# Kernel tuning notes

Hardware: AMD Instinct MI355X
Metric: run time of the kernel (lower is better)

## Reference

```python
import jax, jax.numpy as jnp
import numpy as np

B, T, C, H = 2, 2048, 1024, 16
HD = C // H  # head dim = 64


def setup_inputs() -> dict:
    key = jax.random.key(0)
    ks = jax.random.split(key, 5)
    s = 1.0 / np.sqrt(C)
    return {
        "x": jax.random.normal(ks[0], (B, T, C), dtype=jnp.float32),
        "Wq": jax.random.normal(ks[1], (C, C), dtype=jnp.float32) * s,
        "bq": jnp.zeros((C,), dtype=jnp.float32),
        "Wk": jax.random.normal(ks[2], (C, C), dtype=jnp.float32) * s,
        "bk": jnp.zeros((C,), dtype=jnp.float32),
        "Wv": jax.random.normal(ks[3], (C, C), dtype=jnp.float32) * s,
        "bv": jnp.zeros((C,), dtype=jnp.float32),
        "Wp": jax.random.normal(ks[4], (C, C), dtype=jnp.float32) * s,
        "bp": jnp.zeros((C,), dtype=jnp.float32),
    }


def reference(x, Wq, bq, Wk, bk, Wv, bv, Wp, bp):
    # QKV projections -> [B, H, T, HD]
    def proj(W, b):
        return (x @ W.T + b).reshape(B, T, H, HD).transpose(0, 2, 1, 3)

    q = proj(Wq, bq)
    k = proj(Wk, bk)
    v = proj(Wv, bv)

    scale = 1.0 / np.sqrt(HD)
    att = jnp.einsum("bhtd,bhsd->bhts", q, k) * scale  # [B,H,T,T]
    causal = jnp.tril(jnp.ones((T, T), dtype=bool))
    att = jnp.where(causal, att, -jnp.inf)
    att = jax.nn.softmax(att, axis=-1)
    y = jnp.einsum("bhts,bhsd->bhtd", att, v)          # [B,H,T,HD]
    y = y.transpose(0, 2, 1, 3).reshape(B, T, C)
    return y @ Wp.T + bp
```

## Files before the change

### kernel.cpp

```cpp
#include <hip/hip_runtime.h>
#include <hip/hip_bf16.h>

#define BB 2
#define TT 2048
#define CC 1024
#define HH 16
#define HDD 64

typedef __attribute__((ext_vector_type(8))) short bf16x8;
typedef __attribute__((ext_vector_type(4))) float f32x4;

static __device__ __forceinline__ unsigned short f2bf(float f) {
  union { float f; unsigned u; } v; v.f = f;
  unsigned r = v.u + 0x7fffu + ((v.u >> 16) & 1u);
  return (unsigned short)(r >> 16);
}

static __device__ __forceinline__ unsigned fbits(float f) {
  union { float f; unsigned u; } v; v.f = f; return v.u;
}

static __device__ __forceinline__ unsigned pk_trunc(float lo, float hi) {
  return __builtin_amdgcn_perm(fbits(hi), fbits(lo), 0x07060302u);
}

static __device__ __forceinline__ void gload_lds16(const unsigned short* g, unsigned short* l) {
  __builtin_amdgcn_global_load_lds((const __attribute__((address_space(1))) void*)g,
                                   (__attribute__((address_space(3))) void*)l, 16, 0, 0);
}

__global__ __launch_bounds__(256) void convert_all(
    const float* __restrict__ x, const float* __restrict__ Wq,
    const float* __restrict__ Wk, const float* __restrict__ Wv,
    const float* __restrict__ Wp, unsigned short* __restrict__ dst)
{
  const size_t M4 = 4194304, M1 = 1048576;
  const size_t e = ((size_t)blockIdx.x * 256 + threadIdx.x) * 8;
  const float* src; size_t off;
  if (e < M4)            { src = x;  off = e; }
  else if (e < M4 + M1)  { src = Wq; off = e - M4; }
  else if (e < M4 + 2*M1){ src = Wk; off = e - M4 - M1; }
  else if (e < M4 + 3*M1){ src = Wv; off = e - M4 - 2*M1; }
  else                   { src = Wp; off = e - M4 - 3*M1; }
  float4 a = *(const float4*)(src + off);
  float4 c = *(const float4*)(src + off + 4);
  unsigned short buf[8] = {f2bf(a.x), f2bf(a.y), f2bf(a.z), f2bf(a.w),
                           f2bf(c.x), f2bf(c.y), f2bf(c.z), f2bf(c.w)};
  *(uint4*)(dst + e) = *(const uint4*)buf;
}

__global__ __launch_bounds__(256) void gemm_mfma(
    const unsigned short* __restrict__ A, const unsigned short* __restrict__ W,
    const float* __restrict__ b0, const float* __restrict__ b1, const float* __restrict__ b2,
    unsigned short* __restrict__ oQ, unsigned short* __restrict__ oK,
    unsigned short* __restrict__ oVt)
{
  __shared__ unsigned short As[128][32];
  __shared__ unsigned short Bs[128][32];
  const int t = threadIdx.x;
  const int wv = __builtin_amdgcn_readfirstlane(t >> 6);
  const int ln = t & 63;
  const int l16 = ln & 15;
  const int quad = ln >> 4;
  const int mBase = blockIdx.x * 128;
  const int nBase = blockIdx.y * 128;
  const int wm = (wv >> 1) * 64, wn = (wv & 1) * 64;

  f32x4 acc[4][4];
#pragma unroll
  for (int i = 0; i < 4; i++)
#pragma unroll
    for (int j = 0; j < 4; j++) acc[i][j] = (f32x4){0.f, 0.f, 0.f, 0.f};

  const int ca = wv * 64 + ln;
  const int cb = ca + 256;
  const int ra = ca >> 2, colA = (ca & 3) * 8;
  const int rb = cb >> 2, colB = (cb & 3) * 8;
  unsigned short* ldsA0 = &As[0][0] + (size_t)(wv * 64) * 8;
  unsigned short* ldsA1 = &As[0][0] + (size_t)(256 + wv * 64) * 8;
  unsigned short* ldsB0 = &Bs[0][0] + (size_t)(wv * 64) * 8;
  unsigned short* ldsB1 = &Bs[0][0] + (size_t)(256 + wv * 64) * 8;
  const unsigned short* apA0 = A + (size_t)(mBase + ra) * CC + colA;
  const unsigned short* apA1 = A + (size_t)(mBase + rb) * CC + colB;
  const unsigned short* apB0 = W + (size_t)(nBase + ra) * CC + colA;
  const unsigned short* apB1 = W + (size_t)(nBase + rb) * CC + colB;

  for (int kb = 0; kb < CC; kb += 32) {
    __syncthreads();
    gload_lds16(apA0 + kb, ldsA0);
    gload_lds16(apA1 + kb, ldsA1);
    gload_lds16(apB0 + kb, ldsB0);
    gload_lds16(apB1 + kb, ldsB1);
    __syncthreads();
    bf16x8 af[4], bfr[4];
#pragma unroll
    for (int i = 0; i < 4; i++) af[i] = *(const bf16x8*)&As[wm + i * 16 + l16][quad * 8];
#pragma unroll
    for (int j = 0; j < 4; j++) bfr[j] = *(const bf16x8*)&Bs[wn + j * 16 + l16][quad * 8];
#pragma unroll
    for (int i = 0; i < 4; i++)
#pragma unroll
      for (int j = 0; j < 4; j++)
        acc[i][j] = __builtin_amdgcn_mfma_f32_16x16x32_bf16(af[i], bfr[j], acc[i][j], 0, 0, 0);
  }

  const int which = nBase >> 10;
  if (which < 2) {
    const float* bias = which == 0 ? b0 : b1;
    unsigned short* dst = which == 0 ? oQ : oK;
    const float scl = which == 0 ? 0.1803368801f : 1.0f;
#pragma unroll
    for (int i = 0; i < 4; i++)
#pragma unroll
      for (int r = 0; r < 4; r++) {
        const int m = mBase + wm + i * 16 + quad * 4 + r;
        const int b = m >> 11, tp = m & 2047;
#pragma unroll
        for (int j = 0; j < 4; j++) {
          const int n = nBase + wn + j * 16 + l16;
          const int nl = n & 1023, h = nl >> 6, d = nl & 63;
          dst[((size_t)(b * HH + h) * TT + tp) * HDD + d] =
              f2bf((acc[i][j][r] + bias[nl]) * scl);
        }
      }
  } else {
#pragma unroll
    for (int i = 0; i < 4; i++) {
      const int m0 = mBase + wm + i * 16 + quad * 4;
      const int b = m0 >> 11, tp0 = m0 & 2047;
#pragma unroll
      for (int j = 0; j < 4; j++) {
        const int nl = (nBase + wn + j * 16 + l16) & 1023;
        const int h = nl >> 6, d = nl & 63;
        const float bb = b2[nl];
        unsigned short ph[4];
#pragma unroll
        for (int r = 0; r < 4; r++) ph[r] = f2bf(acc[i][j][r] + bb);
        *(uint2*)&oVt[((size_t)(b * HH + h) * HDD + d) * TT + tp0] = *(const uint2*)ph;
      }
    }
  }
}

__global__ __launch_bounds__(256, 2) void gemm_proj(
    const unsigned short* __restrict__ A, const unsigned short* __restrict__ W,
    const float* __restrict__ bias, float* __restrict__ out)
{
  __shared__ unsigned short As[128][32];
  __shared__ unsigned short Bs[64][32];
  const int t = threadIdx.x;
  const int wv = __builtin_amdgcn_readfirstlane(t >> 6);
  const int ln = t & 63;
  const int l16 = ln & 15;
  const int quad = ln >> 4;
  const int mBase = blockIdx.x * 128;
  const int nBase = blockIdx.y * 64;
  const int wm = (wv >> 1) * 64, wn = (wv & 1) * 32;

  f32x4 acc[4][2];
#pragma unroll
  for (int i = 0; i < 4; i++)
#pragma unroll
    for (int j = 0; j < 2; j++) acc[i][j] = (f32x4){0.f, 0.f, 0.f, 0.f};

  const int ca = wv * 64 + ln;
  const int cb = ca + 256;
  const int ra = ca >> 2, colA = (ca & 3) * 8;
  const int rb = cb >> 2, colB = (cb & 3) * 8;
  unsigned short* ldsA0 = &As[0][0] + (size_t)(wv * 64) * 8;
  unsigned short* ldsA1 = &As[0][0] + (size_t)(256 + wv * 64) * 8;
  unsigned short* ldsB0 = &Bs[0][0] + (size_t)(wv * 64) * 8;
  const unsigned short* apA0 = A + (size_t)(mBase + ra) * CC + colA;
  const unsigned short* apA1 = A + (size_t)(mBase + rb) * CC + colB;
  const unsigned short* apB0 = W + (size_t)(nBase + ra) * CC + colA;

  for (int kb = 0; kb < CC; kb += 32) {
    __syncthreads();
    gload_lds16(apA0 + kb, ldsA0);
    gload_lds16(apA1 + kb, ldsA1);
    gload_lds16(apB0 + kb, ldsB0);
    __syncthreads();
    bf16x8 af[4], bfr[2];
#pragma unroll
    for (int i = 0; i < 4; i++) af[i] = *(const bf16x8*)&As[wm + i * 16 + l16][quad * 8];
#pragma unroll
    for (int j = 0; j < 2; j++) bfr[j] = *(const bf16x8*)&Bs[wn + j * 16 + l16][quad * 8];
#pragma unroll
    for (int i = 0; i < 4; i++)
#pragma unroll
      for (int j = 0; j < 2; j++)
        acc[i][j] = __builtin_amdgcn_mfma_f32_16x16x32_bf16(af[i], bfr[j], acc[i][j], 0, 0, 0);
  }

#pragma unroll
  for (int i = 0; i < 4; i++)
#pragma unroll
    for (int r = 0; r < 4; r++) {
      const int m = mBase + wm + i * 16 + quad * 4 + r;
#pragma unroll
      for (int j = 0; j < 2; j++) {
        const int n = nBase + wn + j * 16 + l16;
        out[(size_t)m * CC + n] = acc[i][j][r] + bias[n];
      }
    }
}

__global__ __launch_bounds__(256, 2) void attn_mfma(
    const unsigned short* __restrict__ Q, const unsigned short* __restrict__ K,
    const unsigned short* __restrict__ Vt, unsigned short* __restrict__ y)
{
  __shared__ unsigned short Qs[128][72];
  __shared__ unsigned short Ks[64][72];
  __shared__ unsigned short Vts[64][72];
  __shared__ unsigned short PtH[4][16][72];
  __shared__ unsigned short PtL[4][16][72];

  const int t = threadIdx.x;
  const int a = blockIdx.x;
  const int bh = blockIdx.y;
  const int wave = t >> 6;
  const int lane = t & 63;
  const int l16 = lane & 15;
  const int quad = lane >> 4;

  const size_t base = (size_t)bh * TT * HDD;
  const int qtL = a, qtH = 31 - a;
  const int qBaseL = qtL * 64, qBaseH = qtH * 64;

#pragma unroll
  for (int p = 0; p < 4; p++) {
    const int c = p * 256 + t;
    const int r = c >> 3, off = (c & 7) * 8;
    const int srcRow = (r < 64) ? (qBaseL + r) : (qBaseH + r - 64);
    *(uint4*)&Qs[r][off] = *(const uint4*)(Q + base + (size_t)srcRow * HDD + off);
  }

  const int sr = t >> 2, sc = (t & 3) * 8;
  const unsigned short* kbase = K + base + (size_t)sr * HDD + sc;
  const unsigned short* vbase = Vt + base + (size_t)sr * TT + sc;
  uint4 kr0 = *(const uint4*)(kbase);
  uint4 kr1 = *(const uint4*)(kbase + 32);
  uint4 vr0 = *(const uint4*)(vbase);
  uint4 vr1 = *(const uint4*)(vbase + 32);
  __syncthreads();

  bf16x8 qfL0 = *(const bf16x8*)&Qs[wave * 16 + l16][quad * 8];
  bf16x8 qfL1 = *(const bf16x8*)&Qs[wave * 16 + l16][32 + quad * 8];
  bf16x8 qfH0 = *(const bf16x8*)&Qs[64 + wave * 16 + l16][quad * 8];
  bf16x8 qfH1 = *(const bf16x8*)&Qs[64 + wave * 16 + l16][32 + quad * 8];

  float lL = 0.f, lH = 0.f;
  f32x4 OfrL[4], OfrH[4];
#pragma unroll
  for (int dt = 0; dt < 4; dt++) {
    OfrL[dt] = (f32x4){0.f, 0.f, 0.f, 0.f};
    OfrH[dt] = (f32x4){0.f, 0.f, 0.f, 0.f};
  }

  for (int kt = 0; kt <= qtH; kt++) {
    *(uint4*)&Ks[sr][sc]       = kr0;
    *(uint4*)&Ks[sr][sc + 32]  = kr1;
    *(uint4*)&Vts[sr][sc]      = vr0;
    *(uint4*)&Vts[sr][sc + 32] = vr1;
    __syncthreads();
    if (kt < qtH) {
      kr0 = *(const uint4*)(kbase + (size_t)(kt + 1) * 64 * HDD);
      kr1 = *(const uint4*)(kbase + (size_t)(kt + 1) * 64 * HDD + 32);
      vr0 = *(const uint4*)(vbase + (kt + 1) * 64);
      vr1 = *(const uint4*)(vbase + (kt + 1) * 64 + 32);
    }
    const bool doLo = (kt <= qtL);

    f32x4 StH[4], StL[4];
#pragma unroll
    for (int ct = 0; ct < 4; ct++) {
      bf16x8 a0 = *(const bf16x8*)&Ks[ct * 16 + l16][quad * 8];
      bf16x8 a1 = *(const bf16x8*)&Ks[ct * 16 + l16][32 + quad * 8];
      f32x4 s = (f32x4){0.f, 0.f, 0.f, 0.f};
      s = __builtin_amdgcn_mfma_f32_16x16x32_bf16(a0, qfH0, s, 0, 0, 0);
      s = __builtin_amdgcn_mfma_f32_16x16x32_bf16(a1, qfH1, s, 0, 0, 0);
      StH[ct] = s;
      if (doLo) {
        f32x4 s2 = (f32x4){0.f, 0.f, 0.f, 0.f};
        s2 = __builtin_amdgcn_mfma_f32_16x16x32_bf16(a0, qfL0, s2, 0, 0, 0);
        s2 = __builtin_amdgcn_mfma_f32_16x16x32_bf16(a1, qfL1, s2, 0, 0, 0);
        StL[ct] = s2;
      }
    }

    const bool diagH = (kt == qtH);
    {
      float lsum = 0.f;
#pragma unroll
      for (int ct = 0; ct < 4; ct++) {
        float p[4];
#pragma unroll
        for (int r = 0; r < 4; r++) {
          float pv = exp2f(StH[ct][r]);
          if (diagH && (ct * 16 + quad * 4 + r > wave * 16 + l16)) pv = 0.f;
          lsum += pv;
          p[r] = pv;
        }
        uint2 pk = {pk_trunc(p[0], p[1]), pk_trunc(p[2], p[3])};
        *(uint2*)&PtH[wave][l16][ct * 16 + quad * 4] = pk;
      }
      lsum += __shfl_xor(lsum, 16, 64);
      lsum += __shfl_xor(lsum, 32, 64);
      lH += lsum;
    }
    if (doLo) {
      const bool diagL = (kt == qtL);
      float lsum = 0.f;
#pragma unroll
      for (int ct = 0; ct < 4; ct++) {
        float p[4];
#pragma unroll
        for (int r = 0; r < 4; r++) {
          float pv = exp2f(StL[ct][r]);
          if (diagL && (ct * 16 + quad * 4 + r > wave * 16 + l16)) pv = 0.f;
          lsum += pv;
          p[r] = pv;
        }
        uint2 pk = {pk_trunc(p[0], p[1]), pk_trunc(p[2], p[3])};
        *(uint2*)&PtL[wave][l16][ct * 16 + quad * 4] = pk;
      }
      lsum += __shfl_xor(lsum, 16, 64);
      lsum += __shfl_xor(lsum, 32, 64);
      lL += lsum;
    }

    bf16x8 paH0 = *(const bf16x8*)&PtH[wave][l16][quad * 8];
    bf16x8 paH1 = *(const bf16x8*)&PtH[wave][l16][32 + quad * 8];
    bf16x8 paL0, paL1;
    if (doLo) {
      paL0 = *(const bf16x8*)&PtL[wave][l16][quad * 8];
      paL1 = *(const bf16x8*)&PtL[wave][l16][32 + quad * 8];
    }
#pragma unroll
    for (int dt = 0; dt < 4; dt++) {
      bf16x8 vb0 = *(const bf16x8*)&Vts[dt * 16 + l16][quad * 8];
      bf16x8 vb1 = *(const bf16x8*)&Vts[dt * 16 + l16][32 + quad * 8];
      OfrH[dt] = __builtin_amdgcn_mfma_f32_16x16x32_bf16(paH0, vb0, OfrH[dt], 0, 0, 0);
      OfrH[dt] = __builtin_amdgcn_mfma_f32_16x16x32_bf16(paH1, vb1, OfrH[dt], 0, 0, 0);
      if (doLo) {
        OfrL[dt] = __builtin_amdgcn_mfma_f32_16x16x32_bf16(paL0, vb0, OfrL[dt], 0, 0, 0);
        OfrL[dt] = __builtin_amdgcn_mfma_f32_16x16x32_bf16(paL1, vb1, OfrL[dt], 0, 0, 0);
      }
    }
    __syncthreads();
  }

  const int b = bh >> 4, h = bh & 15;
  float lRowL[4], lRowH[4];
#pragma unroll
  for (int r = 0; r < 4; r++) {
    lRowL[r] = __shfl(lL, quad * 4 + r, 16);
    lRowH[r] = __shfl(lH, quad * 4 + r, 16);
  }
#pragma unroll
  for (int r = 0; r < 4; r++) {
    const int qL = qBaseL + wave * 16 + quad * 4 + r;
    const int qH = qBaseH + wave * 16 + quad * 4 + r;
    const float invL = 1.0f / lRowL[r];
    const float invH = 1.0f / lRowH[r];
    unsigned short* ypL = y + ((size_t)(b * TT + qL)) * CC + h * 64 + l16;
    unsigned short* ypH = y + ((size_t)(b * TT + qH)) * CC + h * 64 + l16;
#pragma unroll
    for (int dt = 0; dt < 4; dt++) {
      ypL[dt * 16] = f2bf(OfrL[dt][r] * invL);
      ypH[dt * 16] = f2bf(OfrH[dt][r] * invH);
    }
  }
}

extern "C" void kernel_launch(void* const* d_in, const int* in_sizes, int n_in,
                              void* d_out, int out_size, void* d_ws, size_t ws_size,
                              hipStream_t stream) {
  const float* x  = (const float*)d_in[0];
  const float* Wq = (const float*)d_in[1];
  const float* bq = (const float*)d_in[2];
  const float* Wk = (const float*)d_in[3];
  const float* bk = (const float*)d_in[4];
  const float* Wv = (const float*)d_in[5];
  const float* bv = (const float*)d_in[6];
  const float* Wp = (const float*)d_in[7];
  const float* bp = (const float*)d_in[8];

  const size_t M4 = 4194304, M1 = 1048576;
  unsigned short* xb   = (unsigned short*)d_ws;
  unsigned short* wqb  = xb + M4;
  unsigned short* wpb  = wqb + 3 * M1;
  unsigned short* wsQ  = wpb + M1;
  unsigned short* wsK  = wsQ + M4;
  unsigned short* wsVt = wsK + M4;
  unsigned short* yb   = wsVt + M4;

  convert_all<<<4096, 256, 0, stream>>>(x, Wq, Wk, Wv, Wp, xb);
  gemm_mfma<<<dim3(32, 24), 256, 0, stream>>>(xb, wqb, bq, bk, bv,
                                              wsQ, wsK, wsVt);
  attn_mfma<<<dim3(16, BB * HH), 256, 0, stream>>>(wsQ, wsK, wsVt, yb);
  gemm_proj<<<dim3(32, 16), 256, 0, stream>>>(yb, wpb, bp, (float*)d_out);
}
```

Before: 198.8 us.

## Double-buffer attention K/V tiles, shrink proj GEMM tile, unify QKV epilogue

The attention kernel now double-buffers the K/V shared tiles, which removes the trailing barrier per key tile. It reuses the Q staging area for the P scratch, splits the diagonal and non-diagonal softmax paths, and defers the row-sum shuffles to the end. The output projection GEMM moves from 128x64 to 64x64 tiles with twice as many blocks. The QKV epilogue is merged into one path, which turns the V-transposed store from packed 8-byte writes into scalar 2-byte strided writes and may cost store bandwidth.

```diff
diff --git a/kernel.cpp b/kernel.cpp
--- a/kernel.cpp
+++ b/kernel.cpp
@@ -105,95 +105,72 @@
   }
 
   const int which = nBase >> 10;
-  if (which < 2) {
-    const float* bias = which == 0 ? b0 : b1;
-    unsigned short* dst = which == 0 ? oQ : oK;
-    const float scl = which == 0 ? 0.1803368801f : 1.0f;
-#pragma unroll
-    for (int i = 0; i < 4; i++)
-#pragma unroll
-      for (int r = 0; r < 4; r++) {
-        const int m = mBase + wm + i * 16 + quad * 4 + r;
-        const int b = m >> 11, tp = m & 2047;
-#pragma unroll
-        for (int j = 0; j < 4; j++) {
-          const int n = nBase + wn + j * 16 + l16;
-          const int nl = n & 1023, h = nl >> 6, d = nl & 63;
-          dst[((size_t)(b * HH + h) * TT + tp) * HDD + d] =
-              f2bf((acc[i][j][r] + bias[nl]) * scl);
-        }
-      }
-  } else {
-#pragma unroll
-    for (int i = 0; i < 4; i++) {
-      const int m0 = mBase + wm + i * 16 + quad * 4;
-      const int b = m0 >> 11, tp0 = m0 & 2047;
+  const float* bias = which == 0 ? b0 : (which == 1 ? b1 : b2);
+  unsigned short* dst = which == 0 ? oQ : (which == 1 ? oK : oVt);
+  const float scl = which == 0 ? 0.1803368801f : 1.0f;
+#pragma unroll
+  for (int i = 0; i < 4; i++)
+#pragma unroll
+    for (int r = 0; r < 4; r++) {
+      const int m = mBase + wm + i * 16 + quad * 4 + r;
+      const int b = m >> 11, tp = m & 2047;
 #pragma unroll
       for (int j = 0; j < 4; j++) {
-        const int nl = (nBase + wn + j * 16 + l16) & 1023;
-        const int h = nl >> 6, d = nl & 63;
-        const float bb = b2[nl];
-        unsigned short ph[4];
-#pragma unroll
-        for (int r = 0; r < 4; r++) ph[r] = f2bf(acc[i][j][r] + bb);
-        *(uint2*)&oVt[((size_t)(b * HH + h) * HDD + d) * TT + tp0] = *(const uint2*)ph;
-      }
-    }
-  }
-}
-
-__global__ __launch_bounds__(256, 2) void gemm_proj(
+        const int n = nBase + wn + j * 16 + l16;
+        const int nl = n & 1023, h = nl >> 6, d = nl & 63;
+        const unsigned short v = f2bf((acc[i][j][r] + bias[nl]) * scl);
+        if (which < 2) dst[((size_t)(b * HH + h) * TT + tp) * HDD + d] = v;
+        else           dst[((size_t)(b * HH + h) * HDD + d) * TT + tp] = v;
+      }
+    }
+}
+
+__global__ __launch_bounds__(256) void gemm_proj(
     const unsigned short* __restrict__ A, const unsigned short* __restrict__ W,
     const float* __restrict__ bias, float* __restrict__ out)
 {
-  __shared__ unsigned short As[128][32];
+  __shared__ unsigned short As[64][32];
   __shared__ unsigned short Bs[64][32];
   const int t = threadIdx.x;
   const int wv = __builtin_amdgcn_readfirstlane(t >> 6);
   const int ln = t & 63;
   const int l16 = ln & 15;
   const int quad = ln >> 4;
-  const int mBase = blockIdx.x * 128;
+  const int mBase = blockIdx.x * 64;
   const int nBase = blockIdx.y * 64;
-  const int wm = (wv >> 1) * 64, wn = (wv & 1) * 32;
-
-  f32x4 acc[4][2];
-#pragma unroll
-  for (int i = 0; i < 4; i++)
+  const int wm = (wv >> 1) * 32, wn = (wv & 1) * 32;
+
+  f32x4 acc[2][2];
+#pragma unroll
+  for (int i = 0; i < 2; i++)
 #pragma unroll
     for (int j = 0; j < 2; j++) acc[i][j] = (f32x4){0.f, 0.f, 0.f, 0.f};
 
-  const int ca = wv * 64 + ln;
-  const int cb = ca + 256;
-  const int ra = ca >> 2, colA = (ca & 3) * 8;
-  const int rb = cb >> 2, colB = (cb & 3) * 8;
-  unsigned short* ldsA0 = &As[0][0] + (size_t)(wv * 64) * 8;
-  unsigned short* ldsA1 = &As[0][0] + (size_t)(256 + wv * 64) * 8;
-  unsigned short* ldsB0 = &Bs[0][0] + (size_t)(wv * 64) * 8;
-  const unsigned short* apA0 = A + (size_t)(mBase + ra) * CC + colA;
-  const unsigned short* apA1 = A + (size_t)(mBase + rb) * CC + colB;
-  const unsigned short* apB0 = W + (size_t)(nBase + ra) * CC + colA;
+  const int rs = t >> 2, cs = (t & 3) * 8;
+  unsigned short* ldsA = &As[0][0] + (size_t)t * 8;
+  unsigned short* ldsB = &Bs[0][0] + (size_t)t * 8;
+  const unsigned short* apA = A + (size_t)(mBase + rs) * CC + cs;
+  const unsigned short* apB = W + (size_t)(nBase + rs) * CC + cs;
 
   for (int kb = 0; kb < CC; kb += 32) {
     __syncthreads();
-    gload_lds16(apA0 + kb, ldsA0);
-    gload_lds16(apA1 + kb, ldsA1);
-    gload_lds16(apB0 + kb, ldsB0);
+    gload_lds16(apA + kb, ldsA);
+    gload_lds16(apB + kb, ldsB);
     __syncthreads();
-    bf16x8 af[4], bfr[2];
-#pragma unroll
-    for (int i = 0; i < 4; i++) af[i] = *(const bf16x8*)&As[wm + i * 16 + l16][quad * 8];
+    bf16x8 af[2], bfr[2];
+#pragma unroll
+    for (int i = 0; i < 2; i++) af[i] = *(const bf16x8*)&As[wm + i * 16 + l16][quad * 8];
 #pragma unroll
     for (int j = 0; j < 2; j++) bfr[j] = *(const bf16x8*)&Bs[wn + j * 16 + l16][quad * 8];
 #pragma unroll
-    for (int i = 0; i < 4; i++)
+    for (int i = 0; i < 2; i++)
 #pragma unroll
       for (int j = 0; j < 2; j++)
         acc[i][j] = __builtin_amdgcn_mfma_f32_16x16x32_bf16(af[i], bfr[j], acc[i][j], 0, 0, 0);
   }
 
 #pragma unroll
-  for (int i = 0; i < 4; i++)
+  for (int i = 0; i < 2; i++)
 #pragma unroll
     for (int r = 0; r < 4; r++) {
       const int m = mBase + wm + i * 16 + quad * 4 + r;
@@ -209,11 +186,9 @@
     const unsigned short* __restrict__ Q, const unsigned short* __restrict__ K,
     const unsigned short* __restrict__ Vt, unsigned short* __restrict__ y)
 {
-  __shared__ unsigned short Qs[128][72];
-  __shared__ unsigned short Ks[64][72];
-  __shared__ unsigned short Vts[64][72];
-  __shared__ unsigned short PtH[4][16][72];
-  __shared__ unsigned short PtL[4][16][72];
+  __shared__ unsigned short QP[128][72];
+  __shared__ unsigned short Ks[2][64][72];
+  __shared__ unsigned short Vts[2][64][72];
 
   const int t = threadIdx.x;
   const int a = blockIdx.x;
@@ -232,7 +207,7 @@
     const int c = p * 256 + t;
     const int r = c >> 3, off = (c & 7) * 8;
     const int srcRow = (r < 64) ? (qBaseL + r) : (qBaseH + r - 64);
-    *(uint4*)&Qs[r][off] = *(const uint4*)(Q + base + (size_t)srcRow * HDD + off);
+    *(uint4*)&QP[r][off] = *(const uint4*)(Q + base + (size_t)srcRow * HDD + off);
   }
 
   const int sr = t >> 2, sc = (t & 3) * 8;
@@ -244,10 +219,12 @@
   uint4 vr1 = *(const uint4*)(vbase + 32);
   __syncthreads();
 
-  bf16x8 qfL0 = *(const bf16x8*)&Qs[wave * 16 + l16][quad * 8];
-  bf16x8 qfL1 = *(const bf16x8*)&Qs[wave * 16 + l16][32 + quad * 8];
-  bf16x8 qfH0 = *(const bf16x8*)&Qs[64 + wave * 16 + l16][quad * 8];
-  bf16x8 qfH1 = *(const bf16x8*)&Qs[64 + wave * 16 + l16][32 + quad * 8];
+  bf16x8 qfL0 = *(const bf16x8*)&QP[wave * 16 + l16][quad * 8];
+  bf16x8 qfL1 = *(const bf16x8*)&QP[wave * 16 + l16][32 + quad * 8];
+  bf16x8 qfH0 = *(const bf16x8*)&QP[64 + wave * 16 + l16][quad * 8];
+  bf16x8 qfH1 = *(const bf16x8*)&QP[64 + wave * 16 + l16][32 + quad * 8];
+  unsigned short (*PtH)[72] = (unsigned short (*)[72])&QP[wave * 16];
+  unsigned short (*PtL)[72] = (unsigned short (*)[72])&QP[64 + wave * 16];
 
   float lL = 0.f, lH = 0.f;
   f32x4 OfrL[4], OfrH[4];
@@ -258,10 +235,11 @@
   }
 
   for (int kt = 0; kt <= qtH; kt++) {
-    *(uint4*)&Ks[sr][sc]       = kr0;
-    *(uint4*)&Ks[sr][sc + 32]  = kr1;
-    *(uint4*)&Vts[sr][sc]      = vr0;
-    *(uint4*)&Vts[sr][sc + 32] = vr1;
+    const int buf = kt & 1;
+    *(uint4*)&Ks[buf][sr][sc]       = kr0;
+    *(uint4*)&Ks[buf][sr][sc + 32]  = kr1;
+    *(uint4*)&Vts[buf][sr][sc]      = vr0;
+    *(uint4*)&Vts[buf][sr][sc + 32] = vr1;
     __syncthreads();
     if (kt < qtH) {
       kr0 = *(const uint4*)(kbase + (size_t)(kt + 1) * 64 * HDD);
@@ -274,8 +252,8 @@
     f32x4 StH[4], StL[4];
 #pragma unroll
     for (int ct = 0; ct < 4; ct++) {
-      bf16x8 a0 = *(const bf16x8*)&Ks[ct * 16 + l16][quad * 8];
-      bf16x8 a1 = *(const bf16x8*)&Ks[ct * 16 + l16][32 + quad * 8];
+      bf16x8 a0 = *(const bf16x8*)&Ks[buf][ct * 16 + l16][quad * 8];
+      bf16x8 a1 = *(const bf16x8*)&Ks[buf][ct * 16 + l16][32 + quad * 8];
       f32x4 s = (f32x4){0.f, 0.f, 0.f, 0.f};
       s = __builtin_amdgcn_mfma_f32_16x16x32_bf16(a0, qfH0, s, 0, 0, 0);
       s = __builtin_amdgcn_mfma_f32_16x16x32_bf16(a1, qfH1, s, 0, 0, 0);
@@ -288,58 +266,76 @@
       }
     }
 
-    const bool diagH = (kt == qtH);
-    {
-      float lsum = 0.f;
+    if (kt == qtH) {
 #pragma unroll
       for (int ct = 0; ct < 4; ct++) {
         float p[4];
 #pragma unroll
         for (int r = 0; r < 4; r++) {
           float pv = exp2f(StH[ct][r]);
-          if (diagH && (ct * 16 + quad * 4 + r > wave * 16 + l16)) pv = 0.f;
-          lsum += pv;
+          if (ct * 16 + quad * 4 + r > wave * 16 + l16) pv = 0.f;
+          lH += pv;
           p[r] = pv;
         }
         uint2 pk = {pk_trunc(p[0], p[1]), pk_trunc(p[2], p[3])};
-        *(uint2*)&PtH[wave][l16][ct * 16 + quad * 4] = pk;
-      }
-      lsum += __shfl_xor(lsum, 16, 64);
-      lsum += __shfl_xor(lsum, 32, 64);
-      lH += lsum;
-    }
-    if (doLo) {
-      const bool diagL = (kt == qtL);
-      float lsum = 0.f;
+        *(uint2*)&PtH[l16][ct * 16 + quad * 4] = pk;
+      }
+    } else {
 #pragma unroll
       for (int ct = 0; ct < 4; ct++) {
         float p[4];
 #pragma unroll
         for (int r = 0; r < 4; r++) {
-          float pv = exp2f(StL[ct][r]);
-          if (diagL && (ct * 16 + quad * 4 + r > wave * 16 + l16)) pv = 0.f;
-          lsum += pv;
+          const float pv = exp2f(StH[ct][r]);
+          lH += pv;
           p[r] = pv;
         }
         uint2 pk = {pk_trunc(p[0], p[1]), pk_trunc(p[2], p[3])};
-        *(uint2*)&PtL[wave][l16][ct * 16 + quad * 4] = pk;
-      }
-      lsum += __shfl_xor(lsum, 16, 64);
-      lsum += __shfl_xor(lsum, 32, 64);
-      lL += lsum;
-    }
-
-    bf16x8 paH0 = *(const bf16x8*)&PtH[wave][l16][quad * 8];
-    bf16x8 paH1 = *(const bf16x8*)&PtH[wave][l16][32 + quad * 8];
+        *(uint2*)&PtH[l16][ct * 16 + quad * 4] = pk;
+      }
+    }
+    if (doLo) {
+      if (kt == qtL) {
+#pragma unroll
+        for (int ct = 0; ct < 4; ct++) {
+          float p[4];
+#pragma unroll
+          for (int r = 0; r < 4; r++) {
+            float pv = exp2f(StL[ct][r]);
+            if (ct * 16 + quad * 4 + r > wave * 16 + l16) pv = 0.f;
+            lL += pv;
+            p[r] = pv;
+          }
+          uint2 pk = {pk_trunc(p[0], p[1]), pk_trunc(p[2], p[3])};
+          *(uint2*)&PtL[l16][ct * 16 + quad * 4] = pk;
+        }
+      } else {
+#pragma unroll
+        for (int ct = 0; ct < 4; ct++) {
+          float p[4];
+#pragma unroll
+          for (int r = 0; r < 4; r++) {
+            const float pv = exp2f(StL[ct][r]);
+            lL += pv;
+            p[r] = pv;
+          }
+          uint2 pk = {pk_trunc(p[0], p[1]), pk_trunc(p[2], p[3])};
+          *(uint2*)&PtL[l16][ct * 16 + quad * 4] = pk;
+        }
+      }
+    }
+
+    bf16x8 paH0 = *(const bf16x8*)&PtH[l16][quad * 8];
+    bf16x8 paH1 = *(const bf16x8*)&PtH[l16][32 + quad * 8];
     bf16x8 paL0, paL1;
     if (doLo) {
-      paL0 = *(const bf16x8*)&PtL[wave][l16][quad * 8];
-      paL1 = *(const bf16x8*)&PtL[wave][l16][32 + quad * 8];
+      paL0 = *(const bf16x8*)&PtL[l16][quad * 8];
+      paL1 = *(const bf16x8*)&PtL[l16][32 + quad * 8];
     }
 #pragma unroll
     for (int dt = 0; dt < 4; dt++) {
-      bf16x8 vb0 = *(const bf16x8*)&Vts[dt * 16 + l16][quad * 8];
-      bf16x8 vb1 = *(const bf16x8*)&Vts[dt * 16 + l16][32 + quad * 8];
+      bf16x8 vb0 = *(const bf16x8*)&Vts[buf][dt * 16 + l16][quad * 8];
+      bf16x8 vb1 = *(const bf16x8*)&Vts[buf][dt * 16 + l16][32 + quad * 8];
       OfrH[dt] = __builtin_amdgcn_mfma_f32_16x16x32_bf16(paH0, vb0, OfrH[dt], 0, 0, 0);
       OfrH[dt] = __builtin_amdgcn_mfma_f32_16x16x32_bf16(paH1, vb1, OfrH[dt], 0, 0, 0);
       if (doLo) {
@@ -347,8 +343,10 @@
         OfrL[dt] = __builtin_amdgcn_mfma_f32_16x16x32_bf16(paL1, vb1, OfrL[dt], 0, 0, 0);
       }
     }
-    __syncthreads();
-  }
+  }
+
+  lL += __shfl_xor(lL, 16, 64); lL += __shfl_xor(lL, 32, 64);
+  lH += __shfl_xor(lH, 16, 64); lH += __shfl_xor(lH, 32, 64);
 
   const int b = bh >> 4, h = bh & 15;
   float lRowL[4], lRowH[4];
@@ -399,5 +397,5 @@
   gemm_mfma<<<dim3(32, 24), 256, 0, stream>>>(xb, wqb, bq, bk, bv,
                                               wsQ, wsK, wsVt);
   attn_mfma<<<dim3(16, BB * HH), 256, 0, stream>>>(wsQ, wsK, wsVt, yb);
-  gemm_proj<<<dim3(32, 16), 256, 0, stream>>>(yb, wpb, bp, (float*)d_out);
-}
+  gemm_proj<<<dim3(64, 16), 256, 0, stream>>>(yb, wpb, bp, (float*)d_out);
+}
```

Measured after the change: 187.8 us. 5.6% less time.
